# Kernel tuning notes

Measured on AMD Instinct MI355X. Metric: run time of the kernel, lower is better.

## Reference

```python
import jax, jax.numpy as jnp
import numpy as np

B, T, IN, OUT = 8, 2048, 1024, 512
DT, TAU = 1.0, 20.0


def setup_inputs() -> dict:
    key = jax.random.key(0)
    k1, k2 = jax.random.split(key)
    x = jax.random.normal(k1, (B, T, IN), jnp.float32)
    lim = 1.0 / np.sqrt(IN)
    weight = jax.random.uniform(k2, (OUT, IN), jnp.float32, -lim, lim)
    bias = jnp.zeros((OUT,), jnp.float32)
    # fixed tau trainer: decay = exp(-dt / tau) per output feature
    decay = jnp.full((OUT,), float(np.exp(-DT / TAU)), jnp.float32)
    return {"input_tensor": x, "weight": weight, "bias": bias, "decay": decay}


def reference(input_tensor, weight, bias, decay):
    # Hoist the time-invariant GEMM out of the recurrence: [B,T,OUT]
    current = jnp.einsum('bti,oi->bto', input_tensor, weight) + bias
    v0 = jnp.zeros((input_tensor.shape[0], weight.shape[0]), input_tensor.dtype)

    def step(v_tm1, c_t):
        v_t = decay * v_tm1 + (1.0 - decay) * c_t
        return v_t, v_t

    # scan over time axis: [T,B,OUT]
    _, outs = jax.lax.scan(step, v0, jnp.swapaxes(current, 0, 1))
    outputs = jnp.swapaxes(outs, 0, 1)  # [B,T,OUT]
    states = jnp.concatenate([v0[:, None, :], outputs], axis=1)[None]  # [1,B,T+1,OUT]
    return outputs, states
```

## Files before the change

kernel.cpp:

```cpp
#include <hip/hip_runtime.h>
#include <hip/hip_bf16.h>
#include <cstddef>
#include <cstdint>

#define BB    8
#define TT    2048
#define KIN   1024
#define NOUT  512
#define CHUNK 32
#define NCHUNK (TT / CHUNK)

#define BM 128
#define BN 128
#define BK 64
#define NKSTEP (KIN / BK)
#define NPAGE  (KIN / 32)
#define TILEB 8192

typedef __attribute__((ext_vector_type(4))) float          f32x4;
typedef __attribute__((ext_vector_type(4))) unsigned int   u32x4;
typedef _Float16 f16x8 __attribute__((ext_vector_type(8)));

__global__ __launch_bounds__(256) void conv_tiled_f16(
    const float* __restrict__ src, unsigned char* __restrict__ dst, int total) {
  int idx = blockIdx.x * blockDim.x + threadIdx.x;
  const int stride = gridDim.x * blockDim.x;
  for (; idx < total; idx += stride) {
    const int r  = idx >> 7;
    const int s8 = idx & 127;
    const float* p = src + (size_t)r * KIN + s8 * 8;
    float4 a = *reinterpret_cast<const float4*>(p);
    float4 b = *reinterpret_cast<const float4*>(p + 4);
    f16x8 h;
    h[0] = (_Float16)a.x; h[1] = (_Float16)a.y;
    h[2] = (_Float16)a.z; h[3] = (_Float16)a.w;
    h[4] = (_Float16)b.x; h[5] = (_Float16)b.y;
    h[6] = (_Float16)b.z; h[7] = (_Float16)b.w;
    const int row  = r & 127;
    const int page = (r >> 7) * NPAGE + (s8 >> 2);
    const int slot = (s8 & 3) ^ ((row >> 1) & 3);
    *reinterpret_cast<f16x8*>(dst + (size_t)page * TILEB + row * 64 + slot * 16) = h;
  }
}

#define G2L(gp, sp)                                                        \
  __builtin_amdgcn_global_load_lds(                                       \
      (const __attribute__((address_space(1))) void*)(gp),                \
      (__attribute__((address_space(3))) void*)(sp), 16, 0, 0)

__global__ __launch_bounds__(256, 2) void gemm_f16(
    const unsigned char* __restrict__ Xt, const unsigned char* __restrict__ Wt,
    const float* __restrict__ bias, const float* __restrict__ decay,
    unsigned short* __restrict__ Cws, float* __restrict__ vend) {
  __shared__ __align__(16) unsigned char smem[2 * 16384];

  const int tid  = threadIdx.x;
  const int wave = tid >> 6;
  const int lane = tid & 63;
  const int m0 = blockIdx.x * BM;
  const int n0 = blockIdx.y * BN;
  const int wm = (wave >> 1) * 64;
  const int wn = (wave & 1) * 64;
  const int frow = lane & 15;
  const int g    = lane >> 4;

  unsigned char* sA = smem;
  unsigned char* sB = smem + 16384;

  const unsigned char* srcA = Xt + (size_t)(m0 >> 7) * NPAGE * TILEB + tid * 16;
  const unsigned char* srcB = Wt + (size_t)(n0 >> 7) * NPAGE * TILEB + tid * 16;
  const int ldsw = wave * 1024;

  const int swzr = (g ^ ((frow >> 1) & 3)) << 4;

  f32x4 acc[4][4] = {};

  for (int t = 0; t < NKSTEP; ++t) {
    __syncthreads();
    const size_t toff = (size_t)(2 * t) * TILEB;
#pragma unroll
    for (int q = 0; q < 4; ++q) {
      G2L(srcA + toff + q * 4096, sA + q * 4096 + ldsw);
      G2L(srcB + toff + q * 4096, sB + q * 4096 + ldsw);
    }
    __syncthreads();

#pragma unroll
    for (int kk = 0; kk < 2; ++kk) {
      f16x8 af[4];
#pragma unroll
      for (int mi = 0; mi < 4; ++mi)
        af[mi] = *reinterpret_cast<const f16x8*>(
            sA + kk * 8192 + (wm + mi * 16 + frow) * 64 + swzr);
#pragma unroll
      for (int ni = 0; ni < 4; ++ni) {
        f16x8 bf = *reinterpret_cast<const f16x8*>(
            sB + kk * 8192 + (wn + ni * 16 + frow) * 64 + swzr);
#pragma unroll
        for (int mi = 0; mi < 4; ++mi)
          acc[mi][ni] = __builtin_amdgcn_mfma_f32_16x16x32_f16(af[mi], bf, acc[mi][ni], 0, 0, 0);
      }
    }
  }

  const int colb = n0 + wn + frow;
  const int rowb = m0 + wm + (g << 2);
  float bv[4];
#pragma unroll
  for (int ni = 0; ni < 4; ++ni) bv[ni] = bias[colb + ni * 16];
#pragma unroll
  for (int mi = 0; mi < 4; ++mi) {
#pragma unroll
    for (int r = 0; r < 4; ++r) {
#pragma unroll
      for (int ni = 0; ni < 4; ++ni) {
        const _Float16 hv = (_Float16)(acc[mi][ni][r] + bv[ni]);
        Cws[(size_t)(rowb + mi * 16 + r) * NOUT + colb + ni * 16] =
            __builtin_bit_cast(unsigned short, hv);
      }
    }
  }

  {
    float rlo[4], rhi[4];
#pragma unroll
    for (int ni = 0; ni < 4; ++ni) {
      const float d  = decay[colb + ni * 16];
      const float bb = bv[ni];
      const float omd = 1.0f - d;
      const float dd = d * d, d4 = dd * dd, d8 = d4 * d4;
      const float d16 = d8 * d8, d12 = d8 * d4;
      const float dpg = (g == 0) ? d12 : (g == 1) ? d8 : (g == 2) ? d4 : 1.0f;
      float s[4];
#pragma unroll
      for (int mi = 0; mi < 4; ++mi) {
        float v = acc[mi][ni][0] + bb;
        v = v * d + (acc[mi][ni][1] + bb);
        v = v * d + (acc[mi][ni][2] + bb);
        v = v * d + (acc[mi][ni][3] + bb);
        s[mi] = omd * v;
      }
      float ulo = dpg * (s[0] * d16 + s[1]);
      float uhi = dpg * (s[2] * d16 + s[3]);
      ulo += __shfl_xor(ulo, 16); ulo += __shfl_xor(ulo, 32);
      uhi += __shfl_xor(uhi, 16); uhi += __shfl_xor(uhi, 32);
      rlo[ni] = ulo; rhi[ni] = uhi;
    }
    const int b   = m0 >> 11;
    const int clo = ((m0 & (TT - 1)) >> 5) + (wm >> 5);
    const int chunk = clo + (g >> 1);
    const int half  = g >> 1;
    const int nia   = g & 1;
    const float v1 = half ? (nia ? rhi[1] : rhi[0]) : (nia ? rlo[1] : rlo[0]);
    const float v2 = half ? (nia ? rhi[3] : rhi[2]) : (nia ? rlo[3] : rlo[2]);
    const int col1 = n0 + wn + frow + nia * 16;
    float* vp = vend + ((size_t)b * NCHUNK + chunk) * NOUT;
    vp[col1]      = v1;
    vp[col1 + 32] = v2;
  }
}

__global__ __launch_bounds__(256) void gemm_f32_64x64(
    const float* __restrict__ X, const float* __restrict__ W,
    const float* __restrict__ bias, float* __restrict__ C) {
  __shared__ float As[16][65];
  __shared__ float Bs[16][65];
  const int m0  = blockIdx.y * 64;
  const int n0  = blockIdx.x * 64;
  const int tid = threadIdx.x;
  const int tx  = tid & 15;
  const int ty  = tid >> 4;
  const int lr  = tid >> 2;
  const int lk  = (tid & 3) << 2;
  float acc[4][4] = {};
  const float* xa = X + (size_t)(m0 + lr) * KIN + lk;
  const float* wb = W + (size_t)(n0 + lr) * KIN + lk;
  for (int k0 = 0; k0 < KIN; k0 += 16) {
    float4 av = *reinterpret_cast<const float4*>(xa + k0);
    float4 bv = *reinterpret_cast<const float4*>(wb + k0);
    As[lk + 0][lr] = av.x; As[lk + 1][lr] = av.y;
    As[lk + 2][lr] = av.z; As[lk + 3][lr] = av.w;
    Bs[lk + 0][lr] = bv.x; Bs[lk + 1][lr] = bv.y;
    Bs[lk + 2][lr] = bv.z; Bs[lk + 3][lr] = bv.w;
    __syncthreads();
#pragma unroll
    for (int k = 0; k < 16; ++k) {
      float a[4], b[4];
#pragma unroll
      for (int i = 0; i < 4; ++i) a[i] = As[k][ty * 4 + i];
#pragma unroll
      for (int j = 0; j < 4; ++j) b[j] = Bs[k][tx * 4 + j];
#pragma unroll
      for (int i = 0; i < 4; ++i)
#pragma unroll
        for (int j = 0; j < 4; ++j) acc[i][j] += a[i] * b[j];
    }
    __syncthreads();
  }
  const int n = n0 + tx * 4;
  float4 bv = *reinterpret_cast<const float4*>(&bias[n]);
#pragma unroll
  for (int i = 0; i < 4; ++i) {
    const int m = m0 + ty * 4 + i;
    float4 r;
    r.x = acc[i][0] + bv.x; r.y = acc[i][1] + bv.y;
    r.z = acc[i][2] + bv.z; r.w = acc[i][3] + bv.w;
    *reinterpret_cast<float4*>(&C[(size_t)m * NOUT + n]) = r;
  }
}

__global__ __launch_bounds__(512) void scan_fixup2(
    const unsigned short* __restrict__ Cws, const float* __restrict__ vend,
    const float* __restrict__ decay, float* __restrict__ out,
    float* __restrict__ states) {
  const int b = blockIdx.x / NCHUNK;
  const int c = blockIdx.x % NCHUNK;
  const int o = threadIdx.x;
  const float d   = decay[o];
  const float omd = 1.0f - d;
  const float dd = d * d, d4 = dd * dd, d8 = d4 * d4, d16 = d8 * d8;
  const float dL = d16 * d16;

  float v = 0.0f;
  const float* vp = vend + (size_t)b * NCHUNK * NOUT + o;
  for (int cc = 0; cc < c; ++cc) v = dL * v + vp[(size_t)cc * NOUT];

  size_t obase = ((size_t)b * TT + (size_t)c * CHUNK) * NOUT + o;
  size_t sbase = ((size_t)b * (TT + 1) + (size_t)c * CHUNK + 1) * NOUT + o;
#pragma unroll 4
  for (int k = 0; k < CHUNK; ++k) {
    const unsigned short hu = Cws[obase + (size_t)k * NOUT];
    const float cur = (float)__builtin_bit_cast(_Float16, hu);
    v = d * v + omd * cur;
    out[obase + (size_t)k * NOUT]    = v;
    states[sbase + (size_t)k * NOUT] = v;
  }
  if (c == 0) states[((size_t)b * (TT + 1)) * NOUT + o] = 0.0f;
}

__global__ __launch_bounds__(512) void scan_seq(
    float* __restrict__ C, float* __restrict__ states,
    const float* __restrict__ decay) {
  const int b = blockIdx.x;
  const int o = threadIdx.x;
  const float d   = decay[o];
  const float omd = 1.0f - d;
  float v = 0.0f;
  states[((size_t)b * (TT + 1)) * NOUT + o] = 0.0f;
  for (int t = 0; t < TT; ++t) {
    const size_t oi = ((size_t)b * TT + t) * NOUT + o;
    float x = C[oi];
    v = d * v + omd * x;
    C[oi] = v;
    states[((size_t)b * (TT + 1) + t + 1) * NOUT + o] = v;
  }
}

extern "C" void kernel_launch(void* const* d_in, const int* in_sizes, int n_in,
                              void* d_out, int out_size, void* d_ws, size_t ws_size,
                              hipStream_t stream) {
  const float* x     = (const float*)d_in[0];
  const float* w     = (const float*)d_in[1];
  const float* bias  = (const float*)d_in[2];
  const float* decay = (const float*)d_in[3];

  float* out    = (float*)d_out;
  float* states = out + (size_t)BB * TT * NOUT;

  const size_t szXb = (size_t)BB * TT * KIN * sizeof(_Float16);
  const size_t szWb = (size_t)NOUT * KIN * sizeof(_Float16);
  const size_t szCb = (size_t)BB * TT * NOUT * sizeof(_Float16);
  const size_t scan_elems = (size_t)BB * NCHUNK * NOUT;
  const size_t need = szXb + szWb + szCb + scan_elems * sizeof(float);

  if (ws_size >= need) {
    unsigned char*  Xt  = (unsigned char*)d_ws;
    unsigned char*  Wt  = Xt + szXb;
    unsigned short* Cws = (unsigned short*)(Wt + szWb);
    float*          vend = (float*)(Cws + (size_t)BB * TT * NOUT);

    conv_tiled_f16<<<2048, 256, 0, stream>>>(x, Xt, BB * TT * (KIN / 8));
    conv_tiled_f16<<<256,  256, 0, stream>>>(w, Wt, NOUT * (KIN / 8));
    gemm_f16<<<dim3((BB * TT) / BM, NOUT / BN), 256, 0, stream>>>(
        Xt, Wt, bias, decay, Cws, vend);
    scan_fixup2<<<BB * NCHUNK, NOUT, 0, stream>>>(Cws, vend, decay, out, states);
  } else {
    gemm_f32_64x64<<<dim3(NOUT / 64, (BB * TT) / 64), 256, 0, stream>>>(x, w, bias, out);
    scan_seq<<<BB, NOUT, 0, stream>>>(out, states, decay);
  }
}
```

Measured before the change: 69.60 us.

## Fuse fp32-to-fp16 input conversion into GEMM A-tile loads

Drops the separate kernel that converted and tiled the whole 64 MB fp32 input into an fp16 workspace. The GEMM now streams fp32 rows of X straight into LDS through an XOR-swizzled layout and converts each fragment to fp16 in registers with packed round-toward-zero conversion before the MFMA. This removes a full read and write of X plus a kernel launch. In exchange the A tile doubles in LDS (48 KB per block, which may reduce occupancy), global A traffic inside the GEMM doubles since it is fp32 and re-read by every N block, and rounding changes from nearest to toward-zero.

After: 62.16 us. 1.12x faster.

```diff
diff --git a/kernel.cpp b/kernel.cpp
--- a/kernel.cpp
+++ b/kernel.cpp
@@ -49,10 +49,10 @@
       (__attribute__((address_space(3))) void*)(sp), 16, 0, 0)
 
 __global__ __launch_bounds__(256, 2) void gemm_f16(
-    const unsigned char* __restrict__ Xt, const unsigned char* __restrict__ Wt,
+    const float* __restrict__ X, const unsigned char* __restrict__ Wt,
     const float* __restrict__ bias, const float* __restrict__ decay,
     unsigned short* __restrict__ Cws, float* __restrict__ vend) {
-  __shared__ __align__(16) unsigned char smem[2 * 16384];
+  __shared__ __align__(16) unsigned char smem[32768 + 16384];
 
   const int tid  = threadIdx.x;
   const int wave = tid >> 6;
@@ -65,33 +65,49 @@
   const int g    = lane >> 4;
 
   unsigned char* sA = smem;
-  unsigned char* sB = smem + 16384;
-
-  const unsigned char* srcA = Xt + (size_t)(m0 >> 7) * NPAGE * TILEB + tid * 16;
+  unsigned char* sB = smem + 32768;
+
+  const int arow4 = wave * 4 + (lane >> 4);
+  const int aslot = lane & 15;
+  const float* gA = X + (size_t)(m0 + arow4) * KIN + ((aslot ^ (arow4 & 7)) << 2);
+  const int ldsw = wave * 1024;
+
   const unsigned char* srcB = Wt + (size_t)(n0 >> 7) * NPAGE * TILEB + tid * 16;
-  const int ldsw = wave * 1024;
-
-  const int swzr = (g ^ ((frow >> 1) & 3)) << 4;
+
+  const int arswz = frow & 7;
+  const int swzr  = (g ^ ((frow >> 1) & 3)) << 4;
 
   f32x4 acc[4][4] = {};
 
   for (int t = 0; t < NKSTEP; ++t) {
     __syncthreads();
-    const size_t toff = (size_t)(2 * t) * TILEB;
-#pragma unroll
-    for (int q = 0; q < 4; ++q) {
-      G2L(srcA + toff + q * 4096, sA + q * 4096 + ldsw);
-      G2L(srcB + toff + q * 4096, sB + q * 4096 + ldsw);
-    }
+    const int k0 = t * BK;
+#pragma unroll
+    for (int q = 0; q < 8; ++q)
+      G2L(gA + (size_t)(q * 16) * KIN + k0, sA + q * 4096 + ldsw);
+    const size_t boff = (size_t)(2 * t) * TILEB;
+#pragma unroll
+    for (int q = 0; q < 4; ++q)
+      G2L(srcB + boff + q * 4096, sB + q * 4096 + ldsw);
     __syncthreads();
 
 #pragma unroll
     for (int kk = 0; kk < 2; ++kk) {
       f16x8 af[4];
 #pragma unroll
-      for (int mi = 0; mi < 4; ++mi)
-        af[mi] = *reinterpret_cast<const f16x8*>(
-            sA + kk * 8192 + (wm + mi * 16 + frow) * 64 + swzr);
+      for (int mi = 0; mi < 4; ++mi) {
+        const int row = wm + mi * 16 + frow;
+        const unsigned char* ap = sA + row * 256;
+        const int ks0 = kk * 8 + g * 2;
+        f32x4 q0 = *reinterpret_cast<const f32x4*>(ap + ((ks0    ) ^ arswz) * 16);
+        f32x4 q1 = *reinterpret_cast<const f32x4*>(ap + ((ks0 + 1) ^ arswz) * 16);
+        u32x4 hv;
+        hv[0] = __builtin_bit_cast(unsigned int, __builtin_amdgcn_cvt_pkrtz(q0[0], q0[1]));
+        hv[1] = __builtin_bit_cast(unsigned int, __builtin_amdgcn_cvt_pkrtz(q0[2], q0[3]));
+        hv[2] = __builtin_bit_cast(unsigned int, __builtin_amdgcn_cvt_pkrtz(q1[0], q1[1]));
+        hv[3] = __builtin_bit_cast(unsigned int, __builtin_amdgcn_cvt_pkrtz(q1[2], q1[3]));
+        af[mi] = __builtin_bit_cast(f16x8, hv);
+      }
 #pragma unroll
       for (int ni = 0; ni < 4; ++ni) {
         f16x8 bf = *reinterpret_cast<const f16x8*>(
@@ -267,22 +283,19 @@
   float* out    = (float*)d_out;
   float* states = out + (size_t)BB * TT * NOUT;
 
-  const size_t szXb = (size_t)BB * TT * KIN * sizeof(_Float16);
   const size_t szWb = (size_t)NOUT * KIN * sizeof(_Float16);
   const size_t szCb = (size_t)BB * TT * NOUT * sizeof(_Float16);
   const size_t scan_elems = (size_t)BB * NCHUNK * NOUT;
-  const size_t need = szXb + szWb + szCb + scan_elems * sizeof(float);
+  const size_t need = szWb + szCb + scan_elems * sizeof(float);
 
   if (ws_size >= need) {
-    unsigned char*  Xt  = (unsigned char*)d_ws;
-    unsigned char*  Wt  = Xt + szXb;
-    unsigned short* Cws = (unsigned short*)(Wt + szWb);
+    unsigned char*  Wt   = (unsigned char*)d_ws;
+    unsigned short* Cws  = (unsigned short*)(Wt + szWb);
     float*          vend = (float*)(Cws + (size_t)BB * TT * NOUT);
 
-    conv_tiled_f16<<<2048, 256, 0, stream>>>(x, Xt, BB * TT * (KIN / 8));
-    conv_tiled_f16<<<256,  256, 0, stream>>>(w, Wt, NOUT * (KIN / 8));
+    conv_tiled_f16<<<256, 256, 0, stream>>>(w, Wt, NOUT * (KIN / 8));
     gemm_f16<<<dim3((BB * TT) / BM, NOUT / BN), 256, 0, stream>>>(
-        Xt, Wt, bias, decay, Cws, vend);
+        x, Wt, bias, decay, Cws, vend);
     scan_fixup2<<<BB * NCHUNK, NOUT, 0, stream>>>(Cws, vend, decay, out, states);
   } else {
     gemm_f32_64x64<<<dim3(NOUT / 64, (BB * TT) / 64), 256, 0, stream>>>(x, w, bias, out);
```
